# Performance work log

Measured on AMD Instinct MI355X. Metric: run time of the kernel, lower is better.

## Reference

```python
import jax, jax.numpy as jnp
import numpy as np


def conv1x1(x, w, b):
    # x: (B,C,H,W), w: (O,C), b: (O,)
    return jnp.einsum('bchw,oc->bohw', x, w) + b[None, :, None, None]


def maxpool2x2(x):
    B, C, H, W = x.shape
    return x.reshape(B, C, H // 2, 2, W // 2, 2).max(axis=(3, 5))


def setup_inputs() -> dict:
    key = jax.random.key(0)
    ks = jax.random.split(key, 10)
    B, C, H, W = 16, 256, 64, 64
    K = 8
    ck, ch = C // K, C // 2  # 32, 128
    sc = lambda fan_in: 1.0 / np.sqrt(fan_in)
    return {
        'x': jax.random.normal(ks[0], (B, C, H, W), jnp.float32),
        'wf': jax.random.normal(ks[1], (ck, C), jnp.float32) * sc(C),
        'bf': jnp.zeros((ck,), jnp.float32),
        'wg': jax.random.normal(ks[2], (ck, C), jnp.float32) * sc(C),
        'bg': jnp.zeros((ck,), jnp.float32),
        'wh': jax.random.normal(ks[3], (ch, C), jnp.float32) * sc(C),
        'bh': jnp.zeros((ch,), jnp.float32),
        'wv': jax.random.normal(ks[4], (C, ch), jnp.float32) * sc(ch),
        'bv': jnp.zeros((C,), jnp.float32),
        'gamma': jnp.float32(0.5),  # nonzero so the attention branch matters
    }


def reference(x, wf, bf, wg, bg, wh, bh, wv, bv, gamma):
    B, C, H, W = x.shape
    HW = H * W
    f = conv1x1(x, wf, bf).reshape(B, -1, HW)            # (B, C/K, HW)
    g = maxpool2x2(conv1x1(x, wg, bg))                    # (B, C/K, H/2, W/2)
    h = maxpool2x2(conv1x1(x, wh, bh))                    # (B, C/2, H/2, W/2)
    HWp = HW // 4
    g = g.reshape(B, -1, HWp)
    h = h.reshape(B, -1, HWp)
    s = jnp.einsum('bck,bcl->bkl', f, g)                  # (B, HW, HW')
    beta = jax.nn.softmax(s, axis=-1)
    o = jnp.einsum('bjk,blk->bjl', h, beta)               # (B, C/2, HW)
    o = o.reshape(B, -1, H, W)
    return gamma * conv1x1(o, wv, bv) + x
```

## Files before the change

kernel.cpp:

```cpp
#include <hip/hip_runtime.h>
#include <hip/hip_bf16.h>
#include <stdint.h>

#define B_N   16
#define C_N   256
#define W_N   64
#define HW_N  4096
#define CK_N  32
#define CH_N  128
#define HWP_N 1024
#define MR_N  192

typedef __attribute__((ext_vector_type(8))) short short8;
typedef __attribute__((ext_vector_type(4))) float f32x4;
typedef __attribute__((ext_vector_type(4))) unsigned uint4v;

#define MFMA(a, b, c) __builtin_amdgcn_mfma_f32_16x16x32_bf16((a), (b), (c), 0, 0, 0)

__device__ __forceinline__ unsigned short f2bf(float f) {
    union { float f; unsigned u; } v; v.f = f;
    unsigned r = v.u + 0x7FFFu + ((v.u >> 16) & 1u);
    return (unsigned short)(r >> 16);
}
__device__ __forceinline__ unsigned packrn(float lo, float hi) {
    unsigned a = __float_as_uint(lo) + 0x8000u;
    unsigned b = __float_as_uint(hi) + 0x8000u;
    return __builtin_amdgcn_perm(b, a, 0x07060302);
}
__device__ __forceinline__ short8 ld8(const void* p) {
    return *reinterpret_cast<const short8*>(p);
}

__global__ __launch_bounds__(256) void k_prep(
    const float* __restrict__ wf, const float* __restrict__ wg,
    const float* __restrict__ wh, const float* __restrict__ wv,
    unsigned short* __restrict__ Wc, unsigned short* __restrict__ Wv)
{
    int i = blockIdx.x * 256 + threadIdx.x;
    if (i < MR_N * C_N) {
        int r = i / C_N, c = i % C_N;
        float v = (r < 32) ? wf[r * C_N + c]
                : (r < 64) ? wg[(r - 32) * C_N + c]
                           : wh[(r - 64) * C_N + c];
        Wc[i] = f2bf(v);
    }
    if (i < C_N * CH_N) Wv[i] = f2bf(wv[i]);
}

__global__ __launch_bounds__(256) void k_conv_fgh(
    const float* __restrict__ x, const unsigned short* __restrict__ Wc,
    const float* __restrict__ bfp, const float* __restrict__ bgp, const float* __restrict__ bhp,
    unsigned short* __restrict__ f_, unsigned short* __restrict__ g_, unsigned short* __restrict__ h_)
{
    __shared__ __align__(16) unsigned char lds[64 * 512];
    const int T = threadIdx.x;
    const int lane = T & 63, wid = T >> 6;
    const int blk = blockIdx.x;
    const int b = blk >> 6;
    const int seg = blk & 63;
    const int rp = seg >> 1;
    const int half = seg & 1;
    const float* xb = x + (size_t)b * C_N * HW_N;

    #pragma unroll
    for (int i = 0; i < 8; ++i) {
        int task = i * 256 + T;
        int pq = task & 15;
        int cp = task >> 4;
        int px0 = pq * 4;
        int row = 2 * rp + (px0 >> 5);
        int wcol = half * 32 + (px0 & 31);
        const float4 v0 = *reinterpret_cast<const float4*>(xb + (size_t)(2 * cp) * HW_N + row * W_N + wcol);
        const float4 v1 = *reinterpret_cast<const float4*>(xb + (size_t)(2 * cp + 1) * HW_N + row * W_N + wcol);
        float vlo[4] = {v0.x, v0.y, v0.z, v0.w};
        float vhi[4] = {v1.x, v1.y, v1.z, v1.w};
        int kc = cp >> 2, co = cp & 3;
        #pragma unroll
        for (int j = 0; j < 4; ++j) {
            int px = px0 + j;
            *reinterpret_cast<unsigned*>(lds + px * 512 + ((kc ^ (px & 31)) << 4) + co * 4)
                = packrn(vlo[j], vhi[j]);
        }
    }
    __syncthreads();

    const int l15 = lane & 15, quad = lane >> 4;
    f32x4 acc[3][4];
    #pragma unroll
    for (int mt = 0; mt < 3; ++mt)
        #pragma unroll
        for (int nt = 0; nt < 4; ++nt)
            acc[mt][nt] = f32x4{0.f, 0.f, 0.f, 0.f};

    const int m0base = wid * 48;
    for (int k0 = 0; k0 < 256; k0 += 32) {
        short8 afr[3];
        #pragma unroll
        for (int mt = 0; mt < 3; ++mt)
            afr[mt] = ld8(Wc + (size_t)(m0base + mt * 16 + l15) * C_N + k0 + quad * 8);
        #pragma unroll
        for (int nt = 0; nt < 4; ++nt) {
            int px = nt * 16 + l15;
            int kc = (k0 >> 3) + quad;
            short8 bfr = ld8(lds + px * 512 + ((kc ^ (px & 31)) << 4));
            #pragma unroll
            for (int mt = 0; mt < 3; ++mt)
                acc[mt][nt] = MFMA(afr[mt], bfr, acc[mt][nt]);
        }
    }

    #pragma unroll
    for (int mt = 0; mt < 3; ++mt) {
        int mbase = m0base + mt * 16;
        int mrow0 = mbase + quad * 4;
        float bias[4];
        #pragma unroll
        for (int r = 0; r < 4; ++r) {
            int m = mrow0 + r;
            bias[r] = (m < 32) ? bfp[m] : (m < 64) ? bgp[m - 32] : bhp[m - 64];
        }
        if (mbase < 32) {
            #pragma unroll
            for (int nt = 0; nt < 4; ++nt) {
                int px = nt * 16 + l15;
                int p = (2 * rp + (px >> 5)) * W_N + half * 32 + (px & 31);
                uint2 u;
                u.x = packrn(acc[mt][nt][0] + bias[0], acc[mt][nt][1] + bias[1]);
                u.y = packrn(acc[mt][nt][2] + bias[2], acc[mt][nt][3] + bias[3]);
                *reinterpret_cast<uint2*>(f_ + ((size_t)b * HW_N + p) * CK_N + mrow0) = u;
            }
        } else if (mbase < 64) {
            int gc0 = mrow0 - 32;
            #pragma unroll
            for (int nt = 0; nt < 2; ++nt) {
                float pv[4];
                #pragma unroll
                for (int r = 0; r < 4; ++r) {
                    float m1 = fmaxf(acc[mt][nt][r], acc[mt][nt + 2][r]);
                    pv[r] = fmaxf(m1, __shfl_xor(m1, 1)) + bias[r];
                }
                if ((lane & 1) == 0) {
                    int kp = rp * 32 + half * 16 + ((nt * 16 + l15) >> 1);
                    uint2 u;
                    u.x = packrn(pv[0], pv[1]);
                    u.y = packrn(pv[2], pv[3]);
                    *reinterpret_cast<uint2*>(g_ + ((size_t)b * HWP_N + kp) * CK_N + gc0) = u;
                }
            }
        } else {
            int hc0 = mrow0 - 64;
            #pragma unroll
            for (int nt = 0; nt < 2; ++nt) {
                float pv[4];
                #pragma unroll
                for (int r = 0; r < 4; ++r) {
                    float m1 = fmaxf(acc[mt][nt][r], acc[mt][nt + 2][r]);
                    pv[r] = fmaxf(m1, __shfl_xor(m1, 1)) + bias[r];
                }
                #pragma unroll
                for (int r = 0; r < 4; ++r) {
                    int lo = (int)(packrn(pv[r], pv[r]) & 0xFFFFu);
                    int hi = __shfl_down(lo, 2);
                    if ((lane & 3) == 0) {
                        int kp2 = rp * 32 + half * 16 + nt * 8 + (l15 >> 1);
                        *reinterpret_cast<unsigned*>(
                            h_ + ((size_t)b * CH_N + hc0 + r) * HWP_N + kp2)
                            = (unsigned)lo | ((unsigned)hi << 16);
                    }
                }
            }
        }
    }
}

__global__ __launch_bounds__(256, 4) void k_attn(
    const unsigned short* __restrict__ f_, const unsigned short* __restrict__ g_,
    const unsigned short* __restrict__ h_, unsigned short* __restrict__ o_)
{
    __shared__ __align__(16) unsigned char Vl[2 * 17408];
    const int T = threadIdx.x;
    const int lane = T & 63, wid = T >> 6;
    const int l15 = lane & 15, quad = lane >> 4;

    const int blk = blockIdx.x;
    const int b = blk >> 6;
    const int q0w = (blk & 63) * 64 + wid * 16;
    const unsigned short* fb = f_ + (size_t)b * HW_N * CK_N;
    const unsigned short* gb = g_ + (size_t)b * HWP_N * CK_N;
    const unsigned short* hb = h_ + (size_t)b * CH_N * HWP_N;

    short8 ffr = ld8(fb + (size_t)(q0w + l15) * CK_N + quad * 8);

    const f32x4 zf = {0.f, 0.f, 0.f, 0.f};
    f32x4 oacc[8];
    #pragma unroll
    for (int ct = 0; ct < 8; ++ct)
        oacc[ct] = f32x4{0.f, 0.f, 0.f, 0.f};
    float lsum = 0.f;

    const int sch = T >> 3, skq = T & 7;
    const int kq = ((l15 >> 2) << 3) | (l15 & 3);

    uint4 vpre[4];
    #pragma unroll
    for (int i = 0; i < 4; ++i)
        vpre[i] = *reinterpret_cast<const uint4*>(hb + (size_t)(sch + i * 32) * HWP_N + skq * 8);
    short8 gcur[4];
    #pragma unroll
    for (int kt = 0; kt < 4; ++kt)
        gcur[kt] = ld8(gb + (size_t)(((kt >> 1) << 5) + ((kt & 1) << 2) + kq) * CK_N + quad * 8);

    for (int c = 0; c < 16; ++c) {
        unsigned char* buf = Vl + (c & 1) * 17408;
        #pragma unroll
        for (int i = 0; i < 4; ++i) {
            unsigned char* dst = buf + (sch + i * 32) * 136 + skq * 16;
            *reinterpret_cast<uint2*>(dst)     = uint2{vpre[i].x, vpre[i].y};
            *reinterpret_cast<uint2*>(dst + 8) = uint2{vpre[i].z, vpre[i].w};
        }
        if (c < 15) {
            #pragma unroll
            for (int i = 0; i < 4; ++i)
                vpre[i] = *reinterpret_cast<const uint4*>(
                    hb + (size_t)(sch + i * 32) * HWP_N + (c + 1) * 64 + skq * 8);
        }
        __syncthreads();

        f32x4 sp[4];
        #pragma unroll
        for (int kt = 0; kt < 4; ++kt)
            sp[kt] = MFMA(gcur[kt], ffr, zf);
        if (c < 15) {
            #pragma unroll
            for (int kt = 0; kt < 4; ++kt)
                gcur[kt] = ld8(gb + (size_t)((c + 1) * 64 + ((kt >> 1) << 5) + ((kt & 1) << 2) + kq) * CK_N + quad * 8);
        }

        unsigned pw[8];
        float lw = 0.f;
        #pragma unroll
        for (int kt = 0; kt < 4; ++kt) {
            float p0 = __builtin_amdgcn_exp2f(sp[kt][0] * 1.44269504f - 28.85390082f);
            float p1 = __builtin_amdgcn_exp2f(sp[kt][1] * 1.44269504f - 28.85390082f);
            float p2 = __builtin_amdgcn_exp2f(sp[kt][2] * 1.44269504f - 28.85390082f);
            float p3 = __builtin_amdgcn_exp2f(sp[kt][3] * 1.44269504f - 28.85390082f);
            lw += (p0 + p1) + (p2 + p3);
            pw[2 * kt]     = packrn(p0, p1);
            pw[2 * kt + 1] = packrn(p2, p3);
        }
        lsum += lw;
        short8 pfA = __builtin_bit_cast(short8, uint4v{pw[0], pw[1], pw[2], pw[3]});
        short8 pfB = __builtin_bit_cast(short8, uint4v{pw[4], pw[5], pw[6], pw[7]});

        const int vbase = l15 * 136 + quad * 16;
        #pragma unroll
        for (int ct = 0; ct < 8; ++ct) {
            const unsigned char* p = buf + vbase + ct * 2176;
            uint2 aLo0 = *reinterpret_cast<const uint2*>(p);
            uint2 aLo1 = *reinterpret_cast<const uint2*>(p + 8);
            short8 a0 = __builtin_bit_cast(short8, uint4v{aLo0.x, aLo0.y, aLo1.x, aLo1.y});
            oacc[ct] = MFMA(a0, pfA, oacc[ct]);
            uint2 aHi0 = *reinterpret_cast<const uint2*>(p + 64);
            uint2 aHi1 = *reinterpret_cast<const uint2*>(p + 72);
            short8 a1 = __builtin_bit_cast(short8, uint4v{aHi0.x, aHi0.y, aHi1.x, aHi1.y});
            oacc[ct] = MFMA(a1, pfB, oacc[ct]);
        }
    }

    lsum += __shfl_xor(lsum, 16); lsum += __shfl_xor(lsum, 32);
    const float rl = 1.f / lsum;
    unsigned short* ob = o_ + (size_t)b * HW_N * CH_N;
    const int q = q0w + l15;
    #pragma unroll
    for (int ct = 0; ct < 8; ++ct) {
        uint2 u;
        u.x = packrn(oacc[ct][0] * rl, oacc[ct][1] * rl);
        u.y = packrn(oacc[ct][2] * rl, oacc[ct][3] * rl);
        *reinterpret_cast<uint2*>(ob + (size_t)q * CH_N + ct * 16 + quad * 4) = u;
    }
}

__global__ __launch_bounds__(256, 4) void k_out(
    const unsigned short* __restrict__ o_, const unsigned short* __restrict__ Wv,
    const float* __restrict__ bv, const float* __restrict__ x,
    const float* __restrict__ gamma_p, float* __restrict__ out)
{
    const int T = threadIdx.x;
    const int lane = T & 63, wid = T >> 6;
    const int l15 = lane & 15, quad = lane >> 4;
    const int w = blockIdx.x * 4 + wid;
    const int b = w >> 8;
    const int rem = w & 255;
    const int oc0 = (rem >> 6) * 64;
    const int px0 = (rem & 63) * 64;
    const unsigned short* ob = o_ + ((size_t)b * HW_N + px0) * CH_N;

    f32x4 acc[4][4];
    #pragma unroll
    for (int mt = 0; mt < 4; ++mt)
        #pragma unroll
        for (int nt = 0; nt < 4; ++nt)
            acc[mt][nt] = f32x4{0.f, 0.f, 0.f, 0.f};

    #pragma unroll
    for (int k0 = 0; k0 < 128; k0 += 32) {
        short8 bfr[4];
        #pragma unroll
        for (int nt = 0; nt < 4; ++nt)
            bfr[nt] = ld8(ob + (size_t)(nt * 16 + l15) * CH_N + k0 + quad * 8);
        #pragma unroll
        for (int mt = 0; mt < 4; ++mt) {
            short8 afr = ld8(Wv + (size_t)(oc0 + mt * 16 + l15) * CH_N + k0 + quad * 8);
            #pragma unroll
            for (int nt = 0; nt < 4; ++nt)
                acc[mt][nt] = MFMA(bfr[nt], afr, acc[mt][nt]);
        }
    }

    const float gamma = *gamma_p;
    const float* xb = x + (size_t)b * C_N * HW_N;
    float* outb = out + (size_t)b * C_N * HW_N;
    #pragma unroll
    for (int mt = 0; mt < 4; ++mt) {
        int oc = oc0 + mt * 16 + l15;
        float bvv = bv[oc];
        #pragma unroll
        for (int nt = 0; nt < 4; ++nt) {
            size_t base = (size_t)oc * HW_N + px0 + nt * 16 + quad * 4;
            float4 xv = *reinterpret_cast<const float4*>(xb + base);
            float4 ov;
            ov.x = gamma * (acc[mt][nt][0] + bvv) + xv.x;
            ov.y = gamma * (acc[mt][nt][1] + bvv) + xv.y;
            ov.z = gamma * (acc[mt][nt][2] + bvv) + xv.z;
            ov.w = gamma * (acc[mt][nt][3] + bvv) + xv.w;
            *reinterpret_cast<float4*>(outb + base) = ov;
        }
    }
}

extern "C" void kernel_launch(void* const* d_in, const int* in_sizes, int n_in,
                              void* d_out, int out_size, void* d_ws, size_t ws_size,
                              hipStream_t stream) {
    const float* x     = (const float*)d_in[0];
    const float* wf    = (const float*)d_in[1];
    const float* bf    = (const float*)d_in[2];
    const float* wg    = (const float*)d_in[3];
    const float* bg    = (const float*)d_in[4];
    const float* wh    = (const float*)d_in[5];
    const float* bh    = (const float*)d_in[6];
    const float* wv    = (const float*)d_in[7];
    const float* bv    = (const float*)d_in[8];
    const float* gamma = (const float*)d_in[9];
    float* out = (float*)d_out;
    char* ws = (char*)d_ws;

    unsigned short* f_ = (unsigned short*)(ws);
    unsigned short* g_ = (unsigned short*)(ws + 4194304);
    unsigned short* h_ = (unsigned short*)(ws + 5242880);
    unsigned short* o_ = (unsigned short*)(ws + 9437184);
    unsigned short* Wc = (unsigned short*)(ws + 26214400);
    unsigned short* Wv = (unsigned short*)(ws + 26312704);

    k_prep<<<192, 256, 0, stream>>>(wf, wg, wh, wv, Wc, Wv);
    k_conv_fgh<<<1024, 256, 0, stream>>>(x, Wc, bf, bg, bh, f_, g_, h_);
    k_attn<<<1024, 256, 0, stream>>>(f_, g_, h_, o_);
    k_out<<<1024, 256, 0, stream>>>(o_, Wv, bv, x, gamma, out);
}
```

Measured before the change: 206.2 us.

## Fuse output 1x1 conv and residual into attention kernel via LDS

The attention kernel now stages its normalized bf16 output tile in shared memory and immediately applies the value projection conv, bias, gamma scaling and residual add. This removes the separate output kernel and the global round trip of the intermediate o tensor. In exchange the attention kernel carries extra accumulator registers, which may reduce occupancy. It also reuses the shared buffer, which requires the earlier reads to be finished.

```diff
diff --git a/kernel.cpp b/kernel.cpp
--- a/kernel.cpp
+++ b/kernel.cpp
@@ -175,7 +175,9 @@
 
 __global__ __launch_bounds__(256, 4) void k_attn(
     const unsigned short* __restrict__ f_, const unsigned short* __restrict__ g_,
-    const unsigned short* __restrict__ h_, unsigned short* __restrict__ o_)
+    const unsigned short* __restrict__ h_, const unsigned short* __restrict__ Wv,
+    const float* __restrict__ bv, const float* __restrict__ x,
+    const float* __restrict__ gamma_p, float* __restrict__ out)
 {
     __shared__ __align__(16) unsigned char Vl[2 * 17408];
     const int T = threadIdx.x;
@@ -269,51 +271,45 @@
 
     lsum += __shfl_xor(lsum, 16); lsum += __shfl_xor(lsum, 32);
     const float rl = 1.f / lsum;
-    unsigned short* ob = o_ + (size_t)b * HW_N * CH_N;
-    const int q = q0w + l15;
-    #pragma unroll
-    for (int ct = 0; ct < 8; ++ct) {
-        uint2 u;
-        u.x = packrn(oacc[ct][0] * rl, oacc[ct][1] * rl);
-        u.y = packrn(oacc[ct][2] * rl, oacc[ct][3] * rl);
-        *reinterpret_cast<uint2*>(ob + (size_t)q * CH_N + ct * 16 + quad * 4) = u;
-    }
-}
-
-__global__ __launch_bounds__(256, 4) void k_out(
-    const unsigned short* __restrict__ o_, const unsigned short* __restrict__ Wv,
-    const float* __restrict__ bv, const float* __restrict__ x,
-    const float* __restrict__ gamma_p, float* __restrict__ out)
-{
-    const int T = threadIdx.x;
-    const int lane = T & 63, wid = T >> 6;
-    const int l15 = lane & 15, quad = lane >> 4;
-    const int w = blockIdx.x * 4 + wid;
-    const int b = w >> 8;
-    const int rem = w & 255;
-    const int oc0 = (rem >> 6) * 64;
-    const int px0 = (rem & 63) * 64;
-    const unsigned short* ob = o_ + ((size_t)b * HW_N + px0) * CH_N;
-
-    f32x4 acc[4][4];
+
+    unsigned char* o_lds = Vl;
+    {
+        const int row = wid * 16 + l15;
+        #pragma unroll
+        for (int ct = 0; ct < 8; ++ct) {
+            uint2 u;
+            u.x = packrn(oacc[ct][0] * rl, oacc[ct][1] * rl);
+            u.y = packrn(oacc[ct][2] * rl, oacc[ct][3] * rl);
+            *reinterpret_cast<uint2*>(o_lds + row * 264 + (ct * 16 + quad * 4) * 2) = u;
+        }
+    }
+    __syncthreads();
+
+    const int pxb = (blk & 63) * 64;
+    const int oc0 = wid * 64;
+    f32x4 acc2[4][4];
     #pragma unroll
     for (int mt = 0; mt < 4; ++mt)
         #pragma unroll
         for (int nt = 0; nt < 4; ++nt)
-            acc[mt][nt] = f32x4{0.f, 0.f, 0.f, 0.f};
+            acc2[mt][nt] = f32x4{0.f, 0.f, 0.f, 0.f};
 
     #pragma unroll
     for (int k0 = 0; k0 < 128; k0 += 32) {
-        short8 bfr[4];
-        #pragma unroll
-        for (int nt = 0; nt < 4; ++nt)
-            bfr[nt] = ld8(ob + (size_t)(nt * 16 + l15) * CH_N + k0 + quad * 8);
+        short8 ofr[4];
+        #pragma unroll
+        for (int nt = 0; nt < 4; ++nt) {
+            const unsigned char* p = o_lds + (nt * 16 + l15) * 264 + k0 * 2 + quad * 16;
+            uint2 a0 = *reinterpret_cast<const uint2*>(p);
+            uint2 a1 = *reinterpret_cast<const uint2*>(p + 8);
+            ofr[nt] = __builtin_bit_cast(short8, uint4v{a0.x, a0.y, a1.x, a1.y});
+        }
         #pragma unroll
         for (int mt = 0; mt < 4; ++mt) {
-            short8 afr = ld8(Wv + (size_t)(oc0 + mt * 16 + l15) * CH_N + k0 + quad * 8);
+            short8 wfr = ld8(Wv + (size_t)(oc0 + mt * 16 + l15) * CH_N + k0 + quad * 8);
             #pragma unroll
             for (int nt = 0; nt < 4; ++nt)
-                acc[mt][nt] = MFMA(bfr[nt], afr, acc[mt][nt]);
+                acc2[mt][nt] = MFMA(ofr[nt], wfr, acc2[mt][nt]);
         }
     }
 
@@ -326,13 +322,13 @@
         float bvv = bv[oc];
         #pragma unroll
         for (int nt = 0; nt < 4; ++nt) {
-            size_t base = (size_t)oc * HW_N + px0 + nt * 16 + quad * 4;
+            size_t base = (size_t)oc * HW_N + pxb + nt * 16 + quad * 4;
             float4 xv = *reinterpret_cast<const float4*>(xb + base);
             float4 ov;
-            ov.x = gamma * (acc[mt][nt][0] + bvv) + xv.x;
-            ov.y = gamma * (acc[mt][nt][1] + bvv) + xv.y;
-            ov.z = gamma * (acc[mt][nt][2] + bvv) + xv.z;
-            ov.w = gamma * (acc[mt][nt][3] + bvv) + xv.w;
+            ov.x = gamma * (acc2[mt][nt][0] + bvv) + xv.x;
+            ov.y = gamma * (acc2[mt][nt][1] + bvv) + xv.y;
+            ov.z = gamma * (acc2[mt][nt][2] + bvv) + xv.z;
+            ov.w = gamma * (acc2[mt][nt][3] + bvv) + xv.w;
             *reinterpret_cast<float4*>(outb + base) = ov;
         }
     }
@@ -357,12 +353,10 @@
     unsigned short* f_ = (unsigned short*)(ws);
     unsigned short* g_ = (unsigned short*)(ws + 4194304);
     unsigned short* h_ = (unsigned short*)(ws + 5242880);
-    unsigned short* o_ = (unsigned short*)(ws + 9437184);
     unsigned short* Wc = (unsigned short*)(ws + 26214400);
     unsigned short* Wv = (unsigned short*)(ws + 26312704);
 
     k_prep<<<192, 256, 0, stream>>>(wf, wg, wh, wv, Wc, Wv);
     k_conv_fgh<<<1024, 256, 0, stream>>>(x, Wc, bf, bg, bh, f_, g_, h_);
-    k_attn<<<1024, 256, 0, stream>>>(f_, g_, h_, o_);
-    k_out<<<1024, 256, 0, stream>>>(o_, Wv, bv, x, gamma, out);
-}
+    k_attn<<<1024, 256, 0, stream>>>(f_, g_, h_, Wv, bv, x, gamma, out);
+}
```

New measurement: 182.7 us. 11.4% less time.
